# Performance work log

Measured on AMD Instinct MI355X. Metric: run time of the kernel, lower is better.

The kernel has to match this reference:

```python
import jax, jax.numpy as jnp
import numpy as np

L, H, D, DFF, B, S = 4, 8, 512, 2048, 2, 2048
DH = D // H
EPS = 1e-5
SCALE_BASE = 512.0


def setup_inputs() -> dict:
    key = jax.random.key(0)
    ks = jax.random.split(key, 8)
    def w(k, shape, s=0.02):
        return jax.random.normal(k, shape, jnp.float32) * s
    return {
        "x": jax.random.normal(ks[0], (B, S, D), jnp.float32),
        "WQ": w(ks[1], (L, H, D, DH)),
        "WK": w(ks[2], (L, H, D, DH)),
        "WV": w(ks[3], (L, H, D, DH)),
        "WG": w(ks[4], (L, D, D)),
        "WO": w(ks[5], (L, D, D)),
        "gn_w": jnp.ones((L, D), jnp.float32),
        "gn_b": jnp.zeros((L, D), jnp.float32),
        "ln1_w": jnp.ones((L, D), jnp.float32),
        "ln1_b": jnp.zeros((L, D), jnp.float32),
        "ln2_w": jnp.ones((L, D), jnp.float32),
        "ln2_b": jnp.zeros((L, D), jnp.float32),
        "ffn_w1": w(ks[6], (L, D, DFF)),
        "ffn_b1": jnp.zeros((L, DFF), jnp.float32),
        "ffn_w2": w(ks[7], (L, DFF, D)),
        "ffn_b2": jnp.zeros((L, D), jnp.float32),
    }


def _dup(t):
    # duplicate_interleave: [a,b] -> [a,a,b,b]
    return jnp.repeat(t, 2, axis=-1)


def _rot(x):
    # rotate_every_two: (x1,x2) -> (-x2, x1)
    x1, x2 = x[..., ::2], x[..., 1::2]
    return jnp.stack([-x2, x1], axis=-1).reshape(x.shape)


def _xpos(x, downscale):
    # x: [B,H,S,dh]  XPOS rotary with length-extrapolating scale
    s_len, dh = x.shape[-2], x.shape[-1]
    half = dh // 2
    base = (jnp.arange(0, dh, 2, dtype=jnp.float32) + 0.4 * dh) / (1.4 * dh)  # [half]
    power = jnp.arange(s_len, dtype=jnp.float32) / SCALE_BASE
    scale = base[None, :] ** power[:, None]  # [S, half]
    if downscale:
        scale = 1.0 / scale
    inv_freq = 1.0 / (10000.0 ** (jnp.arange(half, dtype=jnp.float32) / half))
    ang = jnp.arange(s_len, dtype=jnp.float32)[:, None] * inv_freq[None, :]
    sin, cos, sc = _dup(jnp.sin(ang)), _dup(jnp.cos(ang)), _dup(scale)
    return x * cos * sc + _rot(x) * sin * sc


def _ln(x, w, b):
    mu = jnp.mean(x, -1, keepdims=True)
    var = jnp.mean((x - mu) ** 2, -1, keepdims=True)
    return (x - mu) * jax.lax.rsqrt(var + EPS) * w + b


def reference(x, WQ, WK, WV, WG, WO, gn_w, gn_b, ln1_w, ln1_b, ln2_w, ln2_b, ffn_w1, ffn_b1, ffn_w2, ffn_b2):
    gammas = 1.0 - jnp.exp(jnp.linspace(np.log(1.0 / 32.0), np.log(1.0 / 512.0), H)).astype(jnp.float32)
    idx = jnp.arange(S, dtype=jnp.float32)
    diff = idx[:, None] - idx[None, :]
    Dmask = jnp.where(diff >= 0, gammas[:, None, None] ** diff, 0.0)  # [H,S,S]
    b = x.shape[0]
    for i in range(L):
        xn = _ln(x, ln1_w[i], ln1_b[i])
        q = _xpos(jnp.einsum('bsd,hde->bhse', xn, WQ[i]), False)
        k = _xpos(jnp.einsum('bsd,hde->bhse', xn, WK[i]), True)
        v = jnp.einsum('bsd,hde->bhse', xn, WV[i])
        att = jnp.einsum('bhse,bhte->bhst', q, k) * Dmask[None]  # [B,H,S,S]
        yh = jnp.einsum('bhst,bhte->bhse', att, v)               # [B,H,S,dh]
        yh = yh.transpose(0, 2, 1, 3)                            # [B,S,H,dh]
        mu = jnp.mean(yh, -1, keepdims=True)
        var = jnp.mean((yh - mu) ** 2, -1, keepdims=True)
        yn = (yh - mu) * jax.lax.rsqrt(var + EPS)
        yn = yn * gn_w[i].reshape(H, DH) + gn_b[i].reshape(H, DH)
        y = yn.reshape(b, S, D)
        g = jax.nn.silu(xn @ WG[i])
        y1 = (g * y) @ WO[i] + x
        h = _ln(y1, ln2_w[i], ln2_b[i])
        x = jax.nn.gelu(h @ ffn_w1[i] + ffn_b1[i], approximate=False) @ ffn_w2[i] + ffn_b2[i] + y1
    return x
```

## Files before the change

### kernel.cpp

```cpp
#include <hip/hip_runtime.h>
#include <hip/hip_bf16.h>

#define LYR 4
#define NH  8
#define DM  512
#define DHD 64
#define DFF 2048
#define BB  2
#define SSL 2048
#define NROWS (BB*SSL)

typedef unsigned short u16;
typedef __attribute__((ext_vector_type(8))) short bf16x8;
typedef __attribute__((ext_vector_type(4))) float f32x4;
typedef __attribute__((ext_vector_type(4))) unsigned int u32x4;

__device__ __forceinline__ u16 f2bf(float f) {
    union { float f; unsigned u; } v; v.f = f;
    unsigned r = v.u + 0x7FFFu + ((v.u >> 16) & 1u);
    return (u16)(r >> 16);
}
__device__ __forceinline__ float bf2f(u16 b) {
    union { unsigned u; float f; } v; v.u = ((unsigned)b) << 16;
    return v.f;
}
__device__ __forceinline__ int swz(int row, int col) {
    return row * 64 + (col & 7) + ((((col >> 3) ^ row) & 7) << 3);
}
__device__ __forceinline__ int swzP(int row, int col) {
    return row * 128 + (col & 7) + ((((col >> 3) ^ row) & 15) << 3);
}
__device__ __forceinline__ void gload16(const u16* g, u16* l) {
    __builtin_amdgcn_global_load_lds(
        (const __attribute__((address_space(1))) unsigned int*)g,
        (__attribute__((address_space(3))) unsigned int*)l, 16, 0, 0);
}
template <int N> __device__ __forceinline__ void wait_vmcnt() {
    if constexpr (N == 0)      asm volatile("s_waitcnt vmcnt(0)" ::: "memory");
    else if constexpr (N == 6) asm volatile("s_waitcnt vmcnt(6)" ::: "memory");
    else if constexpr (N == 8) asm volatile("s_waitcnt vmcnt(8)" ::: "memory");
    else static_assert(N == 0 || N == 6 || N == 8, "unsupported vmcnt");
}
__device__ __forceinline__ void block_barrier() {
    __builtin_amdgcn_s_barrier();
    asm volatile("" ::: "memory");
}


__global__ __launch_bounds__(256) void xpos_tables(float* __restrict__ tab) {
    const int idx = blockIdx.x * 256 + threadIdx.x;
    const int s = idx >> 5, j = idx & 31;
    const float base = (2.f * j + 0.4f * 64.f) / (1.4f * 64.f);
    const float invf = powf(10000.f, -(float)j / 32.f);
    const float ang = (float)s * invf;
    const float scq = powf(base, (float)s / 512.f);
    tab[idx]          = sinf(ang);
    tab[idx + 65536]  = cosf(ang);
    tab[idx + 131072] = scq;
    tab[idx + 196608] = 1.f / scq;
}

__global__ __launch_bounds__(256)
void prep_qkv(const float* __restrict__ WQp, const float* __restrict__ WKp,
              const float* __restrict__ WVp, u16* __restrict__ WBT) {
    const int dt = blockIdx.x;
    const int h = blockIdx.y & 7, which = blockIdx.y >> 3;
    const int l = blockIdx.z;
    const float* W = (which == 0 ? WQp : which == 1 ? WKp : WVp);
    const float* ip = W + ((size_t)(l * 8 + h)) * (512 * 64);
    u16* op = WBT + (size_t)l * (2048 * 512) + (size_t)(which * 512 + h * 64) * 512;
    __shared__ u16 tile[64 * 72];
    const int t = threadIdx.x, rr = t >> 2, cc = (t & 3) * 16;
    const float* src = ip + (size_t)(dt * 64 + rr) * 64 + cc;
#pragma unroll
    for (int i = 0; i < 16; ++i) tile[rr * 72 + cc + i] = f2bf(src[i]);
    __syncthreads();
    u16 tmp[16] __attribute__((aligned(16)));
#pragma unroll
    for (int i = 0; i < 16; ++i) tmp[i] = tile[(cc + i) * 72 + rr];
    u16* dst = op + (size_t)rr * 512 + dt * 64 + cc;
    *(u32x4*)&dst[0] = *(const u32x4*)&tmp[0];
    *(u32x4*)&dst[8] = *(const u32x4*)&tmp[8];
}

__global__ __launch_bounds__(256)
void prep_t(const float* __restrict__ in, u16* __restrict__ out, int R, int C,
            long long in_ls, long long out_ls) {
    const float* ip = in + (size_t)blockIdx.z * in_ls;
    u16* op = out + (size_t)blockIdx.z * out_ls;
    const int r0 = blockIdx.x * 64, c0t = blockIdx.y * 64;
    __shared__ u16 tile[64 * 72];
    const int t = threadIdx.x, rr = t >> 2, cc = (t & 3) * 16;
    const float* src = ip + (size_t)(r0 + rr) * C + c0t + cc;
#pragma unroll
    for (int i = 0; i < 16; ++i) tile[rr * 72 + cc + i] = f2bf(src[i]);
    __syncthreads();
    u16 tmp[16] __attribute__((aligned(16)));
#pragma unroll
    for (int i = 0; i < 16; ++i) tmp[i] = tile[(cc + i) * 72 + rr];
    u16* dst = op + (size_t)(c0t + rr) * R + r0 + cc;
    *(u32x4*)&dst[0] = *(const u32x4*)&tmp[0];
    *(u32x4*)&dst[8] = *(const u32x4*)&tmp[8];
}

__global__ __launch_bounds__(256)
void ln_kernel(const float* __restrict__ x, const float* __restrict__ wt,
               const float* __restrict__ bs, u16* __restrict__ out) {
    const int row = blockIdx.x * 4 + (threadIdx.x >> 6);
    const int lane = threadIdx.x & 63;
    const float* xr = x + (size_t)row * DM + lane * 8;
    float v[8];
    *(float4*)&v[0] = *(const float4*)&xr[0];
    *(float4*)&v[4] = *(const float4*)&xr[4];
    float s = 0.f, s2 = 0.f;
#pragma unroll
    for (int i = 0; i < 8; ++i) { s += v[i]; s2 += v[i] * v[i]; }
#pragma unroll
    for (int m = 1; m < 64; m <<= 1) {
        s  += __shfl_xor(s, m, 64);
        s2 += __shfl_xor(s2, m, 64);
    }
    const float mu = s * (1.f / DM);
    const float rs = rsqrtf(s2 * (1.f / DM) - mu * mu + 1e-5f);
    const int e0 = lane * 8;
    u16 o[8] __attribute__((aligned(16)));
#pragma unroll
    for (int i = 0; i < 8; ++i)
        o[i] = f2bf((v[i] - mu) * rs * wt[e0 + i] + bs[e0 + i]);
    *(u32x4*)&out[(size_t)row * DM + e0] = *(const u32x4*)o;
}

template <int BM, int BN, int EPI>
__global__ __launch_bounds__(256)
void gemm_bt(const u16* __restrict__ A, const u16* __restrict__ Bt,
             u16* __restrict__ obf, float* __restrict__ of32,
             const float* __restrict__ res, const float* __restrict__ bias,
             int M, int N, int K) {
    constexpr int FM = BM / 32, FN = BN / 32;
    constexpr int LPS = BM / 32 + BN / 32;
    __shared__ __align__(16) u16 As[2][BM * 64];
    __shared__ __align__(16) u16 Bs[2][BN * 64];
    const int t = threadIdx.x;
    const int lane = t & 63, w4 = t >> 6;
    const int wr = w4 >> 1, wc = w4 & 1;
    const int fr = lane & 15, fq = lane >> 4;
    const int nX = N / BN;
    const int nwg = (M / BM) * nX;
    const int swzid = (blockIdx.x & 7) * (nwg >> 3) + (blockIdx.x >> 3);
    const int m0 = (swzid / nX) * BM, n0 = (swzid % nX) * BN;
    const int lr = lane >> 3;
    const int ls = lane & 7;
    const int nsteps = K >> 6;

    auto stage = [&](int step, int slot) {
        const int k0 = step << 6;
#pragma unroll
        for (int q = 0; q < BM / 32; ++q) {
            const int ib = q * 4 + w4;
            const int row = ib * 8 + lr;
            const int cc = ls ^ (row & 7);
            gload16(&A[(size_t)(m0 + row) * K + k0 + cc * 8], &As[slot][ib * 512]);
        }
#pragma unroll
        for (int q = 0; q < BN / 32; ++q) {
            const int ib = q * 4 + w4;
            const int row = ib * 8 + lr;
            const int cc = ls ^ (row & 7);
            gload16(&Bt[(size_t)(n0 + row) * K + k0 + cc * 8], &Bs[slot][ib * 512]);
        }
    };

    f32x4 acc[FM][FN] = {};
    stage(0, 0);
    stage(1, 1);
    for (int st = 0; st < nsteps; ++st) {
        if (st + 1 < nsteps) wait_vmcnt<LPS>(); else wait_vmcnt<0>();
        __builtin_amdgcn_sched_barrier(0);
        block_barrier();
        const u16* Ac = As[st & 1];
        const u16* Bc = Bs[st & 1];
#pragma unroll
        for (int ks = 0; ks < 2; ++ks) {
            bf16x8 av[FM], bv[FN];
#pragma unroll
            for (int i = 0; i < FM; ++i)
                av[i] = *(const bf16x8*)&Ac[swz(wr * (BM / 2) + i * 16 + fr, ks * 32 + fq * 8)];
#pragma unroll
            for (int j = 0; j < FN; ++j)
                bv[j] = *(const bf16x8*)&Bc[swz(wc * (BN / 2) + j * 16 + fr, ks * 32 + fq * 8)];
#pragma unroll
            for (int i = 0; i < FM; ++i)
#pragma unroll
                for (int j = 0; j < FN; ++j)
                    acc[i][j] = __builtin_amdgcn_mfma_f32_16x16x32_bf16(av[i], bv[j], acc[i][j], 0, 0, 0);
        }
        asm volatile("s_waitcnt lgkmcnt(0)" ::: "memory");
        __builtin_amdgcn_sched_barrier(0);
        block_barrier();
        if (st + 2 < nsteps) stage(st + 2, st & 1);
    }
#pragma unroll
    for (int i = 0; i < FM; ++i)
#pragma unroll
        for (int j = 0; j < FN; ++j)
#pragma unroll
            for (int r = 0; r < 4; ++r) {
                const int m = m0 + wr * (BM / 2) + i * 16 + fq * 4 + r;
                const int n = n0 + wc * (BN / 2) + j * 16 + fr;
                const size_t idx = (size_t)m * N + n;
                float v = acc[i][j][r];
                if constexpr (EPI == 0) {
                    obf[idx] = f2bf(v);
                } else if constexpr (EPI == 1) {
                    of32[idx] = v + res[idx];
                } else if constexpr (EPI == 2) {
                    float tt = v + bias[n];
                    obf[idx] = f2bf(0.5f * tt * (1.f + erff(tt * 0.7071067811865475f)));
                } else {
                    of32[idx] = v + bias[n] + res[idx];
                }
            }
}

__global__ __launch_bounds__(256)
void xpos_relayout(const u16* __restrict__ qkvg, const float* __restrict__ tab,
                   u16* __restrict__ Qb, u16* __restrict__ Kb, u16* __restrict__ Vt) {
    const int st = blockIdx.x, h = blockIdx.y, b = blockIdx.z;
    const int t = threadIdx.x;
    const int r = t >> 2;
    const int sg = st * 64 + r;
    const size_t rawrow = ((size_t)(b * SSL + sg)) * 2048;
    const size_t qrow = ((size_t)((b * NH + h) * SSL + sg)) * 64;
    const int j0 = (t & 3) * 8;
#pragma unroll
    for (int jj = 0; jj < 8; ++jj) {
        const int j = j0 + jj;
        const float sn = tab[sg * 32 + j];
        const float cs = tab[sg * 32 + j + 65536];
        const float sq = tab[sg * 32 + j + 131072];
        const float sk2 = tab[sg * 32 + j + 196608];
        unsigned rawq = *(const unsigned*)&qkvg[rawrow + h * 64 + 2 * j];
        float q0 = bf2f((u16)(rawq & 0xffff)), q1 = bf2f((u16)(rawq >> 16));
        float o0 = (q0 * cs - q1 * sn) * sq;
        float o1 = (q1 * cs + q0 * sn) * sq;
        *(unsigned*)&Qb[qrow + 2 * j] = ((unsigned)f2bf(o1) << 16) | (unsigned)f2bf(o0);
        unsigned rawk = *(const unsigned*)&qkvg[rawrow + 512 + h * 64 + 2 * j];
        float k0 = bf2f((u16)(rawk & 0xffff)), k1 = bf2f((u16)(rawk >> 16));
        float p0 = (k0 * cs - k1 * sn) * sk2;
        float p1 = (k1 * cs + k0 * sn) * sk2;
        *(unsigned*)&Kb[qrow + 2 * j] = ((unsigned)f2bf(p1) << 16) | (unsigned)f2bf(p0);
    }
    __shared__ __align__(16) u16 vt[64 * 72];
    const int c0 = (t & 3) * 16;
    *(u32x4*)&vt[r * 72 + c0]     = *(const u32x4*)&qkvg[rawrow + 1024 + h * 64 + c0];
    *(u32x4*)&vt[r * 72 + c0 + 8] = *(const u32x4*)&qkvg[rawrow + 1024 + h * 64 + c0 + 8];
    __syncthreads();
    u16 tmp[16] __attribute__((aligned(16)));
#pragma unroll
    for (int i = 0; i < 16; ++i) tmp[i] = vt[(c0 + i) * 72 + r];
    u16* dst = Vt + ((size_t)((b * NH + h) * 64 + r)) * SSL + st * 64 + c0;
    *(u32x4*)&dst[0] = *(const u32x4*)&tmp[0];
    *(u32x4*)&dst[8] = *(const u32x4*)&tmp[8];
}

__global__ __launch_bounds__(512)
void retention(const u16* __restrict__ Qb, const u16* __restrict__ Kb,
               const u16* __restrict__ Vt, const u16* __restrict__ qkvg,
               const float* __restrict__ gnw, const float* __restrict__ gnb,
               u16* __restrict__ zb) {
    extern __shared__ __align__(16) char smem[];
    u16* KsB = (u16*)smem;
    u16* VsB = (u16*)(smem + 32768);
    u16* Qs  = (u16*)(smem + 65536);
    u16* Ps  = (u16*)(smem + 73728);

    const int logical = (blockIdx.x & 7) * 64 + (blockIdx.x >> 3);
    const int bh = logical >> 5;
    const int qt = 31 - (logical & 31);
    const int h = bh & 7, b = bh >> 3;
    const int t = threadIdx.x;
    const int lane = t & 63, w = t >> 6;
    const int fr = lane & 15, fq = lane >> 4;
    const int wr = w & 1, wc2 = w >> 1;
    const int oc = wc2 & 1, th = w >> 2;

    const float gamma = 1.f - expf(-3.4657359f + (float)h * -0.39608410f);
    const float lgam = log2f(gamma);
    const float dlim = 19.931568f / (-lgam);
    const int jt_last = (qt * 64 + 63) >> 7;
    int jt_min = 0;
    {
        const float need = (float)(qt * 64 - 127) - dlim;
        if (need > 0.f) jt_min = (int)ceilf(need * (1.f / 128.f));
        if (jt_min > jt_last) jt_min = jt_last;
        if (jt_min < 0) jt_min = 0;
    }

    float rowf[2][4], colf[2];
#pragma unroll
    for (int i = 0; i < 2; ++i)
#pragma unroll
        for (int rr = 0; rr < 4; ++rr)
            rowf[i][rr] = exp2f((float)(wr * 32 + i * 16 + fq * 4 + rr) * lgam);
#pragma unroll
    for (int j = 0; j < 2; ++j)
        colf[j] = exp2f(-(float)(wc2 * 32 + j * 16 + fr) * lgam);

    const size_t bh2048 = (size_t)bh * 2048;
    const int lr8 = lane >> 3, ls8 = lane & 7;
    const int lr16 = lane >> 4, ls16 = lane & 15;

    {
        const int row = w * 8 + lr8;
        const int cc = ls8 ^ (row & 7);
        gload16(&Qb[(bh2048 + qt * 64 + row) * 64 + cc * 8], &Qs[w * 512]);
    }

    f32x4 oacc[2][2] = {};
    int cur = 0;
    {
        const int jt = jt_min;
        u16* Kd = KsB; u16* Vd = VsB;
#pragma unroll
        for (int q = 0; q < 2; ++q) {
            const int row = q * 64 + w * 8 + lr8;
            const int cc = ls8 ^ (row & 7);
            gload16(&Kb[(bh2048 + jt * 128 + row) * 64 + cc * 8], &Kd[(q * 64 + w * 8) * 64]);
        }
#pragma unroll
        for (int q = 0; q < 2; ++q) {
            const int row = w * 8 + q * 4 + lr16;
            const int cc = ls16 ^ (row & 15);
            gload16(&Vt[((size_t)bh * 64 + row) * 2048 + jt * 128 + cc * 8], &Vd[(w * 8 + q * 4) * 128]);
        }
    }

    for (int jt = jt_min; jt <= jt_last; ++jt) {
        __syncthreads();
        if (jt < jt_last) {
            const int nb = cur ^ 1;
            u16* Kd = KsB + nb * 8192;
            u16* Vd = VsB + nb * 8192;
#pragma unroll
            for (int q = 0; q < 2; ++q) {
                const int row = q * 64 + w * 8 + lr8;
                const int cc = ls8 ^ (row & 7);
                gload16(&Kb[(bh2048 + (jt + 1) * 128 + row) * 64 + cc * 8], &Kd[(q * 64 + w * 8) * 64]);
            }
#pragma unroll
            for (int q = 0; q < 2; ++q) {
                const int row = w * 8 + q * 4 + lr16;
                const int cc = ls16 ^ (row & 15);
                gload16(&Vt[((size_t)bh * 64 + row) * 2048 + (jt + 1) * 128 + cc * 8], &Vd[(w * 8 + q * 4) * 128]);
            }
        }
        const u16* Kc = KsB + cur * 8192;
        f32x4 sac[2][2] = {};
#pragma unroll
        for (int ks = 0; ks < 2; ++ks) {
            bf16x8 qa[2], kb[2];
#pragma unroll
            for (int i = 0; i < 2; ++i)
                qa[i] = *(const bf16x8*)&Qs[swz(wr * 32 + i * 16 + fr, ks * 32 + fq * 8)];
#pragma unroll
            for (int j = 0; j < 2; ++j)
                kb[j] = *(const bf16x8*)&Kc[swz(wc2 * 32 + j * 16 + fr, ks * 32 + fq * 8)];
#pragma unroll
            for (int i = 0; i < 2; ++i)
#pragma unroll
                for (int j = 0; j < 2; ++j)
                    sac[i][j] = __builtin_amdgcn_mfma_f32_16x16x32_bf16(qa[i], kb[j], sac[i][j], 0, 0, 0);
        }
        const float sc = exp2f((float)(qt * 64 - jt * 128) * lgam);
        const bool diag = (jt == jt_last);
#pragma unroll
        for (int i = 0; i < 2; ++i)
#pragma unroll
            for (int j = 0; j < 2; ++j)
#pragma unroll
                for (int rr = 0; rr < 4; ++rr) {
                    float m = sc * rowf[i][rr] * colf[j];
                    if (diag) {
                        const int d = (qt * 64 + wr * 32 + i * 16 + fq * 4 + rr)
                                    - (jt * 128 + wc2 * 32 + j * 16 + fr);
                        if (d < 0) m = 0.f;
                    }
                    Ps[swzP(wr * 32 + i * 16 + fq * 4 + rr, wc2 * 32 + j * 16 + fr)] =
                        f2bf(sac[i][j][rr] * m);
                }
        __syncthreads();
        const u16* Vc = VsB + cur * 8192;
#pragma unroll
        for (int ks = 0; ks < 2; ++ks) {
            const int tcol = th * 64 + ks * 32 + fq * 8;
            bf16x8 pa[2], vb[2];
#pragma unroll
            for (int i = 0; i < 2; ++i)
                pa[i] = *(const bf16x8*)&Ps[swzP(wr * 32 + i * 16 + fr, tcol)];
#pragma unroll
            for (int j = 0; j < 2; ++j)
                vb[j] = *(const bf16x8*)&Vc[swzP(oc * 32 + j * 16 + fr, tcol)];
#pragma unroll
            for (int i = 0; i < 2; ++i)
#pragma unroll
                for (int j = 0; j < 2; ++j)
                    oacc[i][j] = __builtin_amdgcn_mfma_f32_16x16x32_bf16(pa[i], vb[j], oacc[i][j], 0, 0, 0);
        }
        cur ^= 1;
    }

    __syncthreads();
    float* Of = (float*)smem;
    if (th == 1) {
#pragma unroll
        for (int i = 0; i < 2; ++i)
#pragma unroll
            for (int j = 0; j < 2; ++j)
#pragma unroll
                for (int rr = 0; rr < 4; ++rr)
                    Of[(wr * 32 + i * 16 + fq * 4 + rr) * 66 + oc * 32 + j * 16 + fr] = oacc[i][j][rr];
    }
    __syncthreads();
    if (th == 0) {
#pragma unroll
        for (int i = 0; i < 2; ++i)
#pragma unroll
            for (int j = 0; j < 2; ++j)
#pragma unroll
                for (int rr = 0; rr < 4; ++rr) {
                    const int idx = (wr * 32 + i * 16 + fq * 4 + rr) * 66 + oc * 32 + j * 16 + fr;
                    Of[idx] += oacc[i][j][rr];
                }
    }
    __syncthreads();
    const int row = t >> 3, c0 = (t & 7) * 8;
    float v[8];
    float s = 0.f, s2 = 0.f;
#pragma unroll
    for (int i = 0; i < 8; ++i) {
        v[i] = Of[row * 66 + c0 + i];
        s += v[i]; s2 += v[i] * v[i];
    }
    s  += __shfl_xor(s, 1, 64);  s  += __shfl_xor(s, 2, 64);  s  += __shfl_xor(s, 4, 64);
    s2 += __shfl_xor(s2, 1, 64); s2 += __shfl_xor(s2, 2, 64); s2 += __shfl_xor(s2, 4, 64);
    const float mu = s * (1.f / 64.f);
    const float rs = rsqrtf(s2 * (1.f / 64.f) - mu * mu + 1e-5f);
    const int sg = qt * 64 + row;
    u16 gv[8] __attribute__((aligned(16)));
    *(u32x4*)gv = *(const u32x4*)&qkvg[((size_t)(b * SSL + sg)) * 2048 + 1536 + h * 64 + c0];
    u16 ob[8] __attribute__((aligned(16)));
#pragma unroll
    for (int i = 0; i < 8; ++i) {
        const int dc = h * 64 + c0 + i;
        const float yn = (v[i] - mu) * rs * gnw[dc] + gnb[dc];
        const float g = bf2f(gv[i]);
        ob[i] = f2bf(yn * (g / (1.f + expf(-g))));
    }
    *(u32x4*)&zb[((size_t)(b * SSL + sg)) * 512 + h * 64 + c0] = *(const u32x4*)ob;
}

extern "C" void kernel_launch(void* const* d_in, const int* in_sizes, int n_in,
                              void* d_out, int out_size, void* d_ws, size_t ws_size,
                              hipStream_t stream) {
    const float* X    = (const float*)d_in[0];
    const float* WQ   = (const float*)d_in[1];
    const float* WK   = (const float*)d_in[2];
    const float* WV   = (const float*)d_in[3];
    const float* WG   = (const float*)d_in[4];
    const float* WO   = (const float*)d_in[5];
    const float* GNW  = (const float*)d_in[6];
    const float* GNB  = (const float*)d_in[7];
    const float* LN1W = (const float*)d_in[8];
    const float* LN1B = (const float*)d_in[9];
    const float* LN2W = (const float*)d_in[10];
    const float* LN2B = (const float*)d_in[11];
    const float* FW1  = (const float*)d_in[12];
    const float* FB1  = (const float*)d_in[13];
    const float* FW2  = (const float*)d_in[14];
    const float* FB2  = (const float*)d_in[15];

    char* ws = (char*)d_ws;
    size_t off = 0;
    auto alloc = [&](size_t n) { char* p = ws + off; off += (n + 255) & ~(size_t)255; return p; };

    u16*   WBT  = (u16*)alloc((size_t)LYR * 2048 * 512 * 2);
    u16*   WOT  = (u16*)alloc((size_t)LYR * 512 * 512 * 2);
    u16*   W1T  = (u16*)alloc((size_t)LYR * 2048 * 512 * 2);
    u16*   W2T  = (u16*)alloc((size_t)LYR * 512 * 2048 * 2);
    float* TAB  = (float*)alloc((size_t)4 * 2048 * 32 * 4);
    float* XB   = (float*)alloc((size_t)NROWS * DM * 4);
    u16*   XN   = (u16*)alloc((size_t)NROWS * DM * 2);
    u16*   QKVG = (u16*)alloc((size_t)NROWS * 2048 * 2);
    u16*   QBp  = (u16*)alloc((size_t)NROWS * DM * 2);
    u16*   KBp  = (u16*)alloc((size_t)NROWS * DM * 2);
    u16*   VTp  = (u16*)alloc((size_t)NROWS * DM * 2);
    u16*   ZB   = (u16*)alloc((size_t)NROWS * DM * 2);
    float* Y1   = (float*)alloc((size_t)NROWS * DM * 4);
    u16*   HB   = QBp;
    u16*   FF1  = QKVG;

    xpos_tables<<<256, 256, 0, stream>>>(TAB);
    prep_qkv<<<dim3(8, 24, LYR), 256, 0, stream>>>(WQ, WK, WV, WBT);
    prep_t<<<dim3(8, 8, LYR), 256, 0, stream>>>(WG, WBT + 1536 * 512, 512, 512,
                                                (long long)512 * 512, (long long)2048 * 512);
    prep_t<<<dim3(8, 8, LYR), 256, 0, stream>>>(WO, WOT, 512, 512,
                                                (long long)512 * 512, (long long)512 * 512);
    prep_t<<<dim3(8, 32, LYR), 256, 0, stream>>>(FW1, W1T, 512, 2048,
                                                 (long long)512 * 2048, (long long)2048 * 512);
    prep_t<<<dim3(32, 8, LYR), 256, 0, stream>>>(FW2, W2T, 2048, 512,
                                                 (long long)2048 * 512, (long long)512 * 2048);

    for (int l = 0; l < LYR; ++l) {
        const float* xsrc = (l == 0) ? X : XB;
        float* xdst = (l == LYR - 1) ? (float*)d_out : XB;
        ln_kernel<<<NROWS / 4, 256, 0, stream>>>(xsrc, LN1W + l * 512, LN1B + l * 512, XN);
        gemm_bt<128, 128, 0><<<512, 256, 0, stream>>>(
            XN, WBT + (size_t)l * 2048 * 512, QKVG, nullptr, nullptr, nullptr, NROWS, 2048, 512);
        xpos_relayout<<<dim3(SSL / 64, NH, BB), 256, 0, stream>>>(QKVG, TAB, QBp, KBp, VTp);
        retention<<<512, 512, 90112, stream>>>(QBp, KBp, VTp, QKVG,
                                               GNW + l * 512, GNB + l * 512, ZB);
        gemm_bt<64, 128, 1><<<256, 256, 0, stream>>>(
            ZB, WOT + (size_t)l * 512 * 512, nullptr, Y1, xsrc, nullptr, NROWS, 512, 512);
        ln_kernel<<<NROWS / 4, 256, 0, stream>>>(Y1, LN2W + l * 512, LN2B + l * 512, HB);
        gemm_bt<128, 128, 2><<<512, 256, 0, stream>>>(
            HB, W1T + (size_t)l * 2048 * 512, FF1, nullptr, nullptr, FB1 + l * 2048, NROWS, 2048, 512);
        gemm_bt<64, 128, 3><<<256, 256, 0, stream>>>(
            FF1, W2T + (size_t)l * 512 * 2048, nullptr, xdst, Y1, FB2 + l * 512, NROWS, 512, 2048);
    }
}
```

Measured before the change: 475.0 us.

## Replace GEMM with 512-thread 256-wide N tiles and single-prefetch pipeline

Replaces the 256-thread GEMM with a 512-thread version (8 waves in a 2x4 layout) whose N tile is 256 wide, halving the number of workgroups. B fragments are loaded once per k-tile and reused across the M fragments. The pipeline now prefetches only the next tile before computing and waits vmcnt(0) at the end of each step, and MFMA sections run at raised wave priority. Larger tiles improve operand reuse but leave small grids (128 blocks for the N=512 GEMMs) on a 256-CU part, and the shallower prefetch may expose more load latency.

```diff
diff --git a/kernel.cpp b/kernel.cpp
--- a/kernel.cpp
+++ b/kernel.cpp
@@ -34,16 +34,6 @@
     __builtin_amdgcn_global_load_lds(
         (const __attribute__((address_space(1))) unsigned int*)g,
         (__attribute__((address_space(3))) unsigned int*)l, 16, 0, 0);
-}
-template <int N> __device__ __forceinline__ void wait_vmcnt() {
-    if constexpr (N == 0)      asm volatile("s_waitcnt vmcnt(0)" ::: "memory");
-    else if constexpr (N == 6) asm volatile("s_waitcnt vmcnt(6)" ::: "memory");
-    else if constexpr (N == 8) asm volatile("s_waitcnt vmcnt(8)" ::: "memory");
-    else static_assert(N == 0 || N == 6 || N == 8, "unsupported vmcnt");
-}
-__device__ __forceinline__ void block_barrier() {
-    __builtin_amdgcn_s_barrier();
-    asm volatile("" ::: "memory");
 }
 
 
@@ -130,85 +120,92 @@
     *(u32x4*)&out[(size_t)row * DM + e0] = *(const u32x4*)o;
 }
 
-template <int BM, int BN, int EPI>
-__global__ __launch_bounds__(256)
-void gemm_bt(const u16* __restrict__ A, const u16* __restrict__ Bt,
+template <int BM, int EPI>
+__global__ __launch_bounds__(512, 2)
+void gemm_v2(const u16* __restrict__ A, const u16* __restrict__ Bt,
              u16* __restrict__ obf, float* __restrict__ of32,
              const float* __restrict__ res, const float* __restrict__ bias,
              int M, int N, int K) {
-    constexpr int FM = BM / 32, FN = BN / 32;
-    constexpr int LPS = BM / 32 + BN / 32;
+    constexpr int BN = 256;
+    constexpr int FM = BM / 32;
+    constexpr int ART = BM / 64;
     __shared__ __align__(16) u16 As[2][BM * 64];
     __shared__ __align__(16) u16 Bs[2][BN * 64];
     const int t = threadIdx.x;
-    const int lane = t & 63, w4 = t >> 6;
-    const int wr = w4 >> 1, wc = w4 & 1;
+    const int lane = t & 63, w = t >> 6;
+    const int wrm = w >> 2, wcn = w & 3;
     const int fr = lane & 15, fq = lane >> 4;
     const int nX = N / BN;
     const int nwg = (M / BM) * nX;
     const int swzid = (blockIdx.x & 7) * (nwg >> 3) + (blockIdx.x >> 3);
     const int m0 = (swzid / nX) * BM, n0 = (swzid % nX) * BN;
-    const int lr = lane >> 3;
-    const int ls = lane & 7;
-    const int nsteps = K >> 6;
-
-    auto stage = [&](int step, int slot) {
-        const int k0 = step << 6;
-#pragma unroll
-        for (int q = 0; q < BM / 32; ++q) {
-            const int ib = q * 4 + w4;
-            const int row = ib * 8 + lr;
-            const int cc = ls ^ (row & 7);
-            gload16(&A[(size_t)(m0 + row) * K + k0 + cc * 8], &As[slot][ib * 512]);
-        }
-#pragma unroll
-        for (int q = 0; q < BN / 32; ++q) {
-            const int ib = q * 4 + w4;
-            const int row = ib * 8 + lr;
-            const int cc = ls ^ (row & 7);
-            gload16(&Bt[(size_t)(n0 + row) * K + k0 + cc * 8], &Bs[slot][ib * 512]);
+    const int sr = lane >> 3, sg = lane & 7;
+    const int kt = K >> 6;
+
+    auto stage = [&](int tile, int slot) {
+        const int k0 = tile << 6;
+#pragma unroll
+        for (int rb = 0; rb < ART; ++rb) {
+            const int row = rb * 64 + w * 8 + sr;
+            const int cc = sg ^ (row & 7);
+            gload16(&A[(size_t)(m0 + row) * K + k0 + cc * 8],
+                    &As[slot][(rb * 64 + w * 8) * 64]);
+        }
+#pragma unroll
+        for (int rb = 0; rb < 4; ++rb) {
+            const int row = rb * 64 + w * 8 + sr;
+            const int cc = sg ^ (row & 7);
+            gload16(&Bt[(size_t)(n0 + row) * K + k0 + cc * 8],
+                    &Bs[slot][(rb * 64 + w * 8) * 64]);
         }
     };
 
-    f32x4 acc[FM][FN] = {};
+    f32x4 acc[FM][4] = {};
     stage(0, 0);
-    stage(1, 1);
-    for (int st = 0; st < nsteps; ++st) {
-        if (st + 1 < nsteps) wait_vmcnt<LPS>(); else wait_vmcnt<0>();
-        __builtin_amdgcn_sched_barrier(0);
-        block_barrier();
-        const u16* Ac = As[st & 1];
-        const u16* Bc = Bs[st & 1];
-#pragma unroll
-        for (int ks = 0; ks < 2; ++ks) {
-            bf16x8 av[FM], bv[FN];
-#pragma unroll
-            for (int i = 0; i < FM; ++i)
-                av[i] = *(const bf16x8*)&Ac[swz(wr * (BM / 2) + i * 16 + fr, ks * 32 + fq * 8)];
-#pragma unroll
-            for (int j = 0; j < FN; ++j)
-                bv[j] = *(const bf16x8*)&Bc[swz(wc * (BN / 2) + j * 16 + fr, ks * 32 + fq * 8)];
-#pragma unroll
-            for (int i = 0; i < FM; ++i)
-#pragma unroll
-                for (int j = 0; j < FN; ++j)
-                    acc[i][j] = __builtin_amdgcn_mfma_f32_16x16x32_bf16(av[i], bv[j], acc[i][j], 0, 0, 0);
-        }
+    asm volatile("s_waitcnt vmcnt(0)" ::: "memory");
+    __builtin_amdgcn_s_barrier();
+
+    for (int tile = 0; tile < kt; ++tile) {
+        const int s = tile & 1;
+        if (tile + 1 < kt) stage(tile + 1, s ^ 1);
+        const u16* Ac = As[s];
+        const u16* Bc = Bs[s];
+        bf16x8 bv[4][2];
+#pragma unroll
+        for (int j = 0; j < 4; ++j)
+#pragma unroll
+            for (int ks = 0; ks < 2; ++ks)
+                bv[j][ks] = *(const bf16x8*)&Bc[swz(wcn * 64 + j * 16 + fr, ks * 32 + fq * 8)];
+        __builtin_amdgcn_s_setprio(1);
+#pragma unroll
+        for (int q = 0; q < FM; ++q) {
+            const int ar = wrm * (BM / 2) + q * 16 + fr;
+            bf16x8 av0 = *(const bf16x8*)&Ac[swz(ar, fq * 8)];
+            bf16x8 av1 = *(const bf16x8*)&Ac[swz(ar, 32 + fq * 8)];
+#pragma unroll
+            for (int j = 0; j < 4; ++j) {
+                acc[q][j] = __builtin_amdgcn_mfma_f32_16x16x32_bf16(av0, bv[j][0], acc[q][j], 0, 0, 0);
+                acc[q][j] = __builtin_amdgcn_mfma_f32_16x16x32_bf16(av1, bv[j][1], acc[q][j], 0, 0, 0);
+            }
+        }
+        __builtin_amdgcn_s_setprio(0);
         asm volatile("s_waitcnt lgkmcnt(0)" ::: "memory");
         __builtin_amdgcn_sched_barrier(0);
-        block_barrier();
-        if (st + 2 < nsteps) stage(st + 2, st & 1);
-    }
-#pragma unroll
-    for (int i = 0; i < FM; ++i)
-#pragma unroll
-        for (int j = 0; j < FN; ++j)
+        if (tile + 1 < kt)
+            asm volatile("s_waitcnt vmcnt(0)" ::: "memory");
+        __builtin_amdgcn_s_barrier();
+    }
+
+#pragma unroll
+    for (int q = 0; q < FM; ++q)
+#pragma unroll
+        for (int j = 0; j < 4; ++j)
 #pragma unroll
             for (int r = 0; r < 4; ++r) {
-                const int m = m0 + wr * (BM / 2) + i * 16 + fq * 4 + r;
-                const int n = n0 + wc * (BN / 2) + j * 16 + fr;
+                const int m = m0 + wrm * (BM / 2) + q * 16 + fq * 4 + r;
+                const int n = n0 + wcn * 64 + j * 16 + fr;
                 const size_t idx = (size_t)m * N + n;
-                float v = acc[i][j][r];
+                float v = acc[q][j][r];
                 if constexpr (EPI == 0) {
                     obf[idx] = f2bf(v);
                 } else if constexpr (EPI == 1) {
@@ -514,17 +511,17 @@
         const float* xsrc = (l == 0) ? X : XB;
         float* xdst = (l == LYR - 1) ? (float*)d_out : XB;
         ln_kernel<<<NROWS / 4, 256, 0, stream>>>(xsrc, LN1W + l * 512, LN1B + l * 512, XN);
-        gemm_bt<128, 128, 0><<<512, 256, 0, stream>>>(
+        gemm_v2<128, 0><<<256, 512, 0, stream>>>(
             XN, WBT + (size_t)l * 2048 * 512, QKVG, nullptr, nullptr, nullptr, NROWS, 2048, 512);
         xpos_relayout<<<dim3(SSL / 64, NH, BB), 256, 0, stream>>>(QKVG, TAB, QBp, KBp, VTp);
         retention<<<512, 512, 90112, stream>>>(QBp, KBp, VTp, QKVG,
                                                GNW + l * 512, GNB + l * 512, ZB);
-        gemm_bt<64, 128, 1><<<256, 256, 0, stream>>>(
+        gemm_v2<64, 1><<<128, 512, 0, stream>>>(
             ZB, WOT + (size_t)l * 512 * 512, nullptr, Y1, xsrc, nullptr, NROWS, 512, 512);
         ln_kernel<<<NROWS / 4, 256, 0, stream>>>(Y1, LN2W + l * 512, LN2B + l * 512, HB);
-        gemm_bt<128, 128, 2><<<512, 256, 0, stream>>>(
+        gemm_v2<128, 2><<<256, 512, 0, stream>>>(
             HB, W1T + (size_t)l * 2048 * 512, FF1, nullptr, nullptr, FB1 + l * 2048, NROWS, 2048, 512);
-        gemm_bt<64, 128, 3><<<256, 256, 0, stream>>>(
+        gemm_v2<64, 3><<<128, 512, 0, stream>>>(
             FF1, W2T + (size_t)l * 512 * 2048, nullptr, xdst, Y1, FB2 + l * 512, NROWS, 512, 2048);
     }
 }
```

Measured after the change: 535.6 us. 12.8% more time.

## Fuse XPOS rotary and head relayout into the QKVG GEMM epilogue

Applied to the files above, without the earlier changes.

Removes the separate xpos_relayout kernel. The QKVG GEMM now uses 128x64 tiles, so each tile covers exactly one head, and its epilogue applies the XPOS rotation directly into Q/K with lane shuffles. V is transposed through LDS and the gate goes to its own buffer. This avoids writing and re-reading the 4096x2048 bf16 intermediate and one launch per layer. The rotation tables are packed into float4, and the FFN1 GEMM also switches to 128x64 tiles, which adds more workgroups but lowers reuse per tile.

```diff
diff --git a/kernel.cpp b/kernel.cpp
--- a/kernel.cpp
+++ b/kernel.cpp
@@ -47,17 +47,14 @@
 }
 
 
-__global__ __launch_bounds__(256) void xpos_tables(float* __restrict__ tab) {
+__global__ __launch_bounds__(256) void xpos_tables(float4* __restrict__ tab4) {
     const int idx = blockIdx.x * 256 + threadIdx.x;
     const int s = idx >> 5, j = idx & 31;
     const float base = (2.f * j + 0.4f * 64.f) / (1.4f * 64.f);
     const float invf = powf(10000.f, -(float)j / 32.f);
     const float ang = (float)s * invf;
     const float scq = powf(base, (float)s / 512.f);
-    tab[idx]          = sinf(ang);
-    tab[idx + 65536]  = cosf(ang);
-    tab[idx + 131072] = scq;
-    tab[idx + 196608] = 1.f / scq;
+    tab4[idx] = make_float4(sinf(ang), cosf(ang), scq, 1.f / scq);
 }
 
 __global__ __launch_bounds__(256)
@@ -135,9 +132,12 @@
 void gemm_bt(const u16* __restrict__ A, const u16* __restrict__ Bt,
              u16* __restrict__ obf, float* __restrict__ of32,
              const float* __restrict__ res, const float* __restrict__ bias,
+             u16* __restrict__ qb, u16* __restrict__ kb, u16* __restrict__ vt,
+             u16* __restrict__ gb, const float4* __restrict__ tab4,
              int M, int N, int K) {
     constexpr int FM = BM / 32, FN = BN / 32;
     constexpr int LPS = BM / 32 + BN / 32;
+    static_assert(LPS == 6, "vmcnt template expects 6");
     __shared__ __align__(16) u16 As[2][BM * 64];
     __shared__ __align__(16) u16 Bs[2][BN * 64];
     const int t = threadIdx.x;
@@ -199,73 +199,91 @@
         block_barrier();
         if (st + 2 < nsteps) stage(st + 2, st & 1);
     }
-#pragma unroll
-    for (int i = 0; i < FM; ++i)
-#pragma unroll
-        for (int j = 0; j < FN; ++j)
-#pragma unroll
-            for (int r = 0; r < 4; ++r) {
-                const int m = m0 + wr * (BM / 2) + i * 16 + fq * 4 + r;
-                const int n = n0 + wc * (BN / 2) + j * 16 + fr;
-                const size_t idx = (size_t)m * N + n;
-                float v = acc[i][j][r];
-                if constexpr (EPI == 0) {
-                    obf[idx] = f2bf(v);
-                } else if constexpr (EPI == 1) {
-                    of32[idx] = v + res[idx];
-                } else if constexpr (EPI == 2) {
-                    float tt = v + bias[n];
-                    obf[idx] = f2bf(0.5f * tt * (1.f + erff(tt * 0.7071067811865475f)));
-                } else {
-                    of32[idx] = v + bias[n] + res[idx];
+
+    if constexpr (EPI == 4) {
+        const int region = n0 >> 9;
+        const int h = (n0 & 511) >> 6;
+        const int b = m0 >> 11;
+        const int bh = b * NH + h;
+        const int s0 = m0 & 2047;
+        if (region == 3) {
+#pragma unroll
+            for (int i = 0; i < FM; ++i)
+#pragma unroll
+                for (int j = 0; j < FN; ++j)
+#pragma unroll
+                    for (int r = 0; r < 4; ++r) {
+                        const int m = m0 + wr * (BM / 2) + i * 16 + fq * 4 + r;
+                        const int e = wc * (BN / 2) + j * 16 + fr;
+                        gb[(size_t)m * 512 + h * 64 + e] = f2bf(acc[i][j][r]);
+                    }
+        } else if (region <= 1) {
+            u16* dst = (region == 0) ? qb : kb;
+#pragma unroll
+            for (int i = 0; i < FM; ++i)
+#pragma unroll
+                for (int j = 0; j < FN; ++j)
+#pragma unroll
+                    for (int r = 0; r < 4; ++r) {
+                        const int s = s0 + wr * (BM / 2) + i * 16 + fq * 4 + r;
+                        const int e = wc * (BN / 2) + j * 16 + fr;
+                        const float v = acc[i][j][r];
+                        const float p = __shfl_xor(v, 1, 64);
+                        const float rot = (e & 1) ? p : -p;
+                        const float4 t4 = tab4[(size_t)s * 32 + (e >> 1)];
+                        const float scl = (region == 0) ? t4.z : t4.w;
+                        dst[((size_t)bh * 2048 + s) * 64 + e] =
+                            f2bf((v * t4.y + rot * t4.x) * scl);
+                    }
+        } else {
+            constexpr int LTS = BM + 8;
+            u16* LT = (u16*)As;
+#pragma unroll
+            for (int i = 0; i < FM; ++i)
+#pragma unroll
+                for (int j = 0; j < FN; ++j)
+#pragma unroll
+                    for (int r = 0; r < 4; ++r) {
+                        const int sl = wr * (BM / 2) + i * 16 + fq * 4 + r;
+                        const int e = wc * (BN / 2) + j * 16 + fr;
+                        LT[e * LTS + sl] = f2bf(acc[i][j][r]);
+                    }
+            __syncthreads();
+            for (int c = t; c < 64 * (BM / 8); c += 256) {
+                const int er = c / (BM / 8);
+                const int sc = (c % (BM / 8)) * 8;
+                const u32x4 vrow = *(const u32x4*)&LT[er * LTS + sc];
+                *(u32x4*)&vt[((size_t)bh * 64 + er) * 2048 + s0 + sc] = vrow;
+            }
+        }
+    } else {
+#pragma unroll
+        for (int i = 0; i < FM; ++i)
+#pragma unroll
+            for (int j = 0; j < FN; ++j)
+#pragma unroll
+                for (int r = 0; r < 4; ++r) {
+                    const int m = m0 + wr * (BM / 2) + i * 16 + fq * 4 + r;
+                    const int n = n0 + wc * (BN / 2) + j * 16 + fr;
+                    const size_t idx = (size_t)m * N + n;
+                    float v = acc[i][j][r];
+                    if constexpr (EPI == 0) {
+                        obf[idx] = f2bf(v);
+                    } else if constexpr (EPI == 1) {
+                        of32[idx] = v + res[idx];
+                    } else if constexpr (EPI == 2) {
+                        float tt = v + bias[n];
+                        obf[idx] = f2bf(0.5f * tt * (1.f + erff(tt * 0.7071067811865475f)));
+                    } else {
+                        of32[idx] = v + bias[n] + res[idx];
+                    }
                 }
-            }
-}
-
-__global__ __launch_bounds__(256)
-void xpos_relayout(const u16* __restrict__ qkvg, const float* __restrict__ tab,
-                   u16* __restrict__ Qb, u16* __restrict__ Kb, u16* __restrict__ Vt) {
-    const int st = blockIdx.x, h = blockIdx.y, b = blockIdx.z;
-    const int t = threadIdx.x;
-    const int r = t >> 2;
-    const int sg = st * 64 + r;
-    const size_t rawrow = ((size_t)(b * SSL + sg)) * 2048;
-    const size_t qrow = ((size_t)((b * NH + h) * SSL + sg)) * 64;
-    const int j0 = (t & 3) * 8;
-#pragma unroll
-    for (int jj = 0; jj < 8; ++jj) {
-        const int j = j0 + jj;
-        const float sn = tab[sg * 32 + j];
-        const float cs = tab[sg * 32 + j + 65536];
-        const float sq = tab[sg * 32 + j + 131072];
-        const float sk2 = tab[sg * 32 + j + 196608];
-        unsigned rawq = *(const unsigned*)&qkvg[rawrow + h * 64 + 2 * j];
-        float q0 = bf2f((u16)(rawq & 0xffff)), q1 = bf2f((u16)(rawq >> 16));
-        float o0 = (q0 * cs - q1 * sn) * sq;
-        float o1 = (q1 * cs + q0 * sn) * sq;
-        *(unsigned*)&Qb[qrow + 2 * j] = ((unsigned)f2bf(o1) << 16) | (unsigned)f2bf(o0);
-        unsigned rawk = *(const unsigned*)&qkvg[rawrow + 512 + h * 64 + 2 * j];
-        float k0 = bf2f((u16)(rawk & 0xffff)), k1 = bf2f((u16)(rawk >> 16));
-        float p0 = (k0 * cs - k1 * sn) * sk2;
-        float p1 = (k1 * cs + k0 * sn) * sk2;
-        *(unsigned*)&Kb[qrow + 2 * j] = ((unsigned)f2bf(p1) << 16) | (unsigned)f2bf(p0);
-    }
-    __shared__ __align__(16) u16 vt[64 * 72];
-    const int c0 = (t & 3) * 16;
-    *(u32x4*)&vt[r * 72 + c0]     = *(const u32x4*)&qkvg[rawrow + 1024 + h * 64 + c0];
-    *(u32x4*)&vt[r * 72 + c0 + 8] = *(const u32x4*)&qkvg[rawrow + 1024 + h * 64 + c0 + 8];
-    __syncthreads();
-    u16 tmp[16] __attribute__((aligned(16)));
-#pragma unroll
-    for (int i = 0; i < 16; ++i) tmp[i] = vt[(c0 + i) * 72 + r];
-    u16* dst = Vt + ((size_t)((b * NH + h) * 64 + r)) * SSL + st * 64 + c0;
-    *(u32x4*)&dst[0] = *(const u32x4*)&tmp[0];
-    *(u32x4*)&dst[8] = *(const u32x4*)&tmp[8];
+    }
 }
 
 __global__ __launch_bounds__(512)
 void retention(const u16* __restrict__ Qb, const u16* __restrict__ Kb,
-               const u16* __restrict__ Vt, const u16* __restrict__ qkvg,
+               const u16* __restrict__ Vt, const u16* __restrict__ gate,
                const float* __restrict__ gnw, const float* __restrict__ gnb,
                u16* __restrict__ zb) {
     extern __shared__ __align__(16) char smem[];
@@ -358,18 +376,18 @@
         f32x4 sac[2][2] = {};
 #pragma unroll
         for (int ks = 0; ks < 2; ++ks) {
-            bf16x8 qa[2], kb[2];
+            bf16x8 qa[2], kb2[2];
 #pragma unroll
             for (int i = 0; i < 2; ++i)
                 qa[i] = *(const bf16x8*)&Qs[swz(wr * 32 + i * 16 + fr, ks * 32 + fq * 8)];
 #pragma unroll
             for (int j = 0; j < 2; ++j)
-                kb[j] = *(const bf16x8*)&Kc[swz(wc2 * 32 + j * 16 + fr, ks * 32 + fq * 8)];
+                kb2[j] = *(const bf16x8*)&Kc[swz(wc2 * 32 + j * 16 + fr, ks * 32 + fq * 8)];
 #pragma unroll
             for (int i = 0; i < 2; ++i)
 #pragma unroll
                 for (int j = 0; j < 2; ++j)
-                    sac[i][j] = __builtin_amdgcn_mfma_f32_16x16x32_bf16(qa[i], kb[j], sac[i][j], 0, 0, 0);
+                    sac[i][j] = __builtin_amdgcn_mfma_f32_16x16x32_bf16(qa[i], kb2[j], sac[i][j], 0, 0, 0);
         }
         const float sc = exp2f((float)(qt * 64 - jt * 128) * lgam);
         const bool diag = (jt == jt_last);
@@ -447,7 +465,7 @@
     const float rs = rsqrtf(s2 * (1.f / 64.f) - mu * mu + 1e-5f);
     const int sg = qt * 64 + row;
     u16 gv[8] __attribute__((aligned(16)));
-    *(u32x4*)gv = *(const u32x4*)&qkvg[((size_t)(b * SSL + sg)) * 2048 + 1536 + h * 64 + c0];
+    *(u32x4*)gv = *(const u32x4*)&gate[((size_t)(b * SSL + sg)) * 512 + h * 64 + c0];
     u16 ob[8] __attribute__((aligned(16)));
 #pragma unroll
     for (int i = 0; i < 8; ++i) {
@@ -487,19 +505,19 @@
     u16*   WOT  = (u16*)alloc((size_t)LYR * 512 * 512 * 2);
     u16*   W1T  = (u16*)alloc((size_t)LYR * 2048 * 512 * 2);
     u16*   W2T  = (u16*)alloc((size_t)LYR * 512 * 2048 * 2);
-    float* TAB  = (float*)alloc((size_t)4 * 2048 * 32 * 4);
+    float4* TAB4 = (float4*)alloc((size_t)2048 * 32 * 16);
     float* XB   = (float*)alloc((size_t)NROWS * DM * 4);
     u16*   XN   = (u16*)alloc((size_t)NROWS * DM * 2);
-    u16*   QKVG = (u16*)alloc((size_t)NROWS * 2048 * 2);
+    u16*   FF1  = (u16*)alloc((size_t)NROWS * 2048 * 2);
+    u16*   GB   = (u16*)alloc((size_t)NROWS * DM * 2);
     u16*   QBp  = (u16*)alloc((size_t)NROWS * DM * 2);
     u16*   KBp  = (u16*)alloc((size_t)NROWS * DM * 2);
     u16*   VTp  = (u16*)alloc((size_t)NROWS * DM * 2);
     u16*   ZB   = (u16*)alloc((size_t)NROWS * DM * 2);
     float* Y1   = (float*)alloc((size_t)NROWS * DM * 4);
     u16*   HB   = QBp;
-    u16*   FF1  = QKVG;
-
-    xpos_tables<<<256, 256, 0, stream>>>(TAB);
+
+    xpos_tables<<<256, 256, 0, stream>>>(TAB4);
     prep_qkv<<<dim3(8, 24, LYR), 256, 0, stream>>>(WQ, WK, WV, WBT);
     prep_t<<<dim3(8, 8, LYR), 256, 0, stream>>>(WG, WBT + 1536 * 512, 512, 512,
                                                 (long long)512 * 512, (long long)2048 * 512);
@@ -514,17 +532,20 @@
         const float* xsrc = (l == 0) ? X : XB;
         float* xdst = (l == LYR - 1) ? (float*)d_out : XB;
         ln_kernel<<<NROWS / 4, 256, 0, stream>>>(xsrc, LN1W + l * 512, LN1B + l * 512, XN);
-        gemm_bt<128, 128, 0><<<512, 256, 0, stream>>>(
-            XN, WBT + (size_t)l * 2048 * 512, QKVG, nullptr, nullptr, nullptr, NROWS, 2048, 512);
-        xpos_relayout<<<dim3(SSL / 64, NH, BB), 256, 0, stream>>>(QKVG, TAB, QBp, KBp, VTp);
-        retention<<<512, 512, 90112, stream>>>(QBp, KBp, VTp, QKVG,
+        gemm_bt<128, 64, 4><<<1024, 256, 0, stream>>>(
+            XN, WBT + (size_t)l * 2048 * 512, nullptr, nullptr, nullptr, nullptr,
+            QBp, KBp, VTp, GB, TAB4, NROWS, 2048, 512);
+        retention<<<512, 512, 90112, stream>>>(QBp, KBp, VTp, GB,
                                                GNW + l * 512, GNB + l * 512, ZB);
         gemm_bt<64, 128, 1><<<256, 256, 0, stream>>>(
-            ZB, WOT + (size_t)l * 512 * 512, nullptr, Y1, xsrc, nullptr, NROWS, 512, 512);
+            ZB, WOT + (size_t)l * 512 * 512, nullptr, Y1, xsrc, nullptr,
+            nullptr, nullptr, nullptr, nullptr, nullptr, NROWS, 512, 512);
         ln_kernel<<<NROWS / 4, 256, 0, stream>>>(Y1, LN2W + l * 512, LN2B + l * 512, HB);
-        gemm_bt<128, 128, 2><<<512, 256, 0, stream>>>(
-            HB, W1T + (size_t)l * 2048 * 512, FF1, nullptr, nullptr, FB1 + l * 2048, NROWS, 2048, 512);
+        gemm_bt<128, 64, 2><<<1024, 256, 0, stream>>>(
+            HB, W1T + (size_t)l * 2048 * 512, FF1, nullptr, nullptr, FB1 + l * 2048,
+            nullptr, nullptr, nullptr, nullptr, nullptr, NROWS, 2048, 512);
         gemm_bt<64, 128, 3><<<256, 256, 0, stream>>>(
-            FF1, W2T + (size_t)l * 512 * 2048, nullptr, xdst, Y1, FB2 + l * 512, NROWS, 512, 2048);
-    }
-}
+            FF1, W2T + (size_t)l * 512 * 2048, nullptr, xdst, Y1, FB2 + l * 512,
+            nullptr, nullptr, nullptr, nullptr, nullptr, NROWS, 512, 2048);
+    }
+}
```

Result: no change. 477.3 us (+0.5%).
